# Optimization experiments

Hardware: AMD Instinct MI355X
Metric: run time of the kernel (lower is better)

Reference implementation:

```python
import jax, jax.numpy as jnp
import numpy as np

VOL = 128
FACTOR = 0.5 * VOL
N = 262144
LAT = 16
B = 8


def setup_inputs() -> dict:
    key = jax.random.key(0)
    ks = jax.random.split(key, 10)
    x = jax.random.normal(ks[0], (B, LAT), jnp.float32)
    inds = jax.random.randint(ks[1], (N, 3), 1, 126, dtype=jnp.int32)
    reference_values = jax.random.normal(ks[2], (N,), jnp.float32)
    # SIREN first layer: U(-1/in, 1/in)
    W0 = jax.random.uniform(ks[3], (LAT, 8), jnp.float32, -1.0 / LAT, 1.0 / LAT)
    b0 = jnp.zeros((8,), jnp.float32)
    # SIREN hidden layers (4 residual layers): U(-sqrt(6/in), sqrt(6/in))
    lim_h = float(np.sqrt(6.0 / 8.0))
    Wh = jax.random.uniform(ks[4], (4, 8, 8), jnp.float32, -lim_h, lim_h)
    bh = jnp.zeros((4, 8), jnp.float32)
    # final glorot-uniform layer: 8 -> 4N
    lim_f = float(np.sqrt(6.0 / (8.0 + 4.0 * N)))
    Wf = jax.random.uniform(ks[5], (8, 4 * N), jnp.float32, -lim_f, lim_f)
    bf = jnp.zeros((4 * N,), jnp.float32)
    return {"x": x, "W0": W0, "b0": b0, "Wh": Wh, "bh": bh, "Wf": Wf,
            "bf": bf, "reference_values": reference_values, "inds": inds}


def _siren_mlp(x, W0, b0, Wh, bh, Wf, bf):
    bf16 = jnp.bfloat16
    h = jnp.sin(30.0 * (x.astype(bf16) @ W0.astype(bf16) + b0.astype(bf16)))
    for i in range(Wh.shape[0]):  # 4 residual sine layers, 8-wide
        h = h + jnp.sin(h @ Wh[i].astype(bf16) + bh[i].astype(bf16))
    return h.astype(jnp.float32) @ Wf + bf  # [B, 4N], final layer in fp32


def reference(x, W0, b0, Wh, bh, Wf, bf, reference_values, inds):
    Bn = x.shape[0]
    out = _siren_mlp(x, W0, b0, Wh, bh, Wf, bf).reshape(Bn, N, 4)
    delta_coords, delta_values = out[..., :3], out[..., 3]
    # coords = stack(z,y,x reversed) normalized to [-1,1)
    coords_norm = (jnp.stack([inds[:, 2], inds[:, 1], inds[:, 0]], axis=1)
                   .astype(jnp.float32) - FACTOR) / FACTOR  # [N,3]
    values = reference_values + delta_values                 # [B,N]
    coords = FACTOR * (coords_norm[None] + delta_coords) + FACTOR  # [B,N,3]
    bposf = jnp.floor(coords)
    bposi = bposf.astype(jnp.int32)
    f = coords - bposf
    fx, fy, fz = f[..., 0], f[..., 1], f[..., 2]
    gx, gy, gz = 1.0 - fx, 1.0 - fy, 1.0 - fz
    # 8 trilinear weights, in the original concat order
    w = jnp.stack([gx * gy * gz, fx * gy * gz, gx * fy * gz, gx * gy * fz,
                   gx * fy * fz, fx * gy * fz, fx * fy * gz, fx * fy * fz],
                  axis=1)                                    # [B,8,N]
    bamp = (values[:, None, :] * w).reshape(Bn, 8 * N)
    offs = jnp.array([[0, 0, 0], [1, 0, 0], [0, 1, 0], [0, 0, 1],
                      [0, 1, 1], [1, 0, 1], [1, 1, 0], [1, 1, 1]], jnp.int32)
    bpos = (bposi[:, None, :, :] + offs[None, :, None, :]).reshape(Bn, 8 * N, 3)

    def scatter(pos, amp):
        return jnp.zeros((VOL, VOL, VOL), jnp.float32).at[
            pos[:, 2], pos[:, 1], pos[:, 0]].add(amp)

    grids = jax.vmap(scatter)(bpos, bamp)  # [B,128,128,128]
    return grids
```

## Files before the change

kernel.cpp:

```cpp
#include <hip/hip_runtime.h>
#include <math.h>

#define VOL   128
#define V2    (VOL*VOL)
#define V3    (VOL*VOL*VOL)
#define NPTS  262144
#define LATD  16
#define BATCH 8
#define FACTORF 64.0f
#define NBINS (VOL*VOL)
#define RZ 8
#define RY 4
#define REG_PER_B ((VOL/RZ)*(VOL/RY))
#define HALO_Z 13
#define HALO_Y 9
#define NRANGE (HALO_Z*HALO_Y)
#define FAR_CAP 8192

#define WS_HBUF    0u
#define WS_HIST    256u
#define WS_START   65792u
#define WS_RANK    131344u
#define WS_WGSUM   1179920u
#define WS_CTRL    1180432u
#define WS_FARLIST 1180464u
#define WS_COORDS  1737008u
#define WS_FULL    35291440u

__device__ __forceinline__ float bf16r(float x) {
    unsigned u = __float_as_uint(x);
    u = (u + 0x7fffu + ((u >> 16) & 1u)) & 0xffff0000u;
    return __uint_as_float(u);
}

__global__ void mlp_kernel(const float* __restrict__ x,
                           const float* __restrict__ W0,
                           const float* __restrict__ b0,
                           const float* __restrict__ Wh,
                           const float* __restrict__ bh,
                           float* __restrict__ hout) {
    int b = threadIdx.x;
    if (b >= BATCH) return;
    float xb[LATD];
    #pragma unroll
    for (int i = 0; i < LATD; ++i) xb[i] = bf16r(x[b*LATD + i]);
    float h[8];
    #pragma unroll
    for (int j = 0; j < 8; ++j) {
        float acc = 0.f;
        #pragma unroll
        for (int i = 0; i < LATD; ++i) acc += xb[i] * bf16r(W0[i*8 + j]);
        float t = bf16r(acc);
        t = bf16r(t + bf16r(b0[j]));
        t = bf16r(30.0f * t);
        h[j] = bf16r(sinf(t));
    }
    for (int l = 0; l < 4; ++l) {
        float nh[8];
        #pragma unroll
        for (int j = 0; j < 8; ++j) {
            float acc = 0.f;
            #pragma unroll
            for (int r = 0; r < 8; ++r) acc += h[r] * bf16r(Wh[(l*8 + r)*8 + j]);
            float t = bf16r(acc);
            t = bf16r(t + bf16r(bh[l*8 + j]));
            float s = bf16r(sinf(t));
            nh[j] = bf16r(h[j] + s);
        }
        #pragma unroll
        for (int j = 0; j < 8; ++j) h[j] = nh[j];
    }
    #pragma unroll
    for (int j = 0; j < 8; ++j) hout[b*8 + j] = h[j];
}

__global__ __launch_bounds__(256) void hist_rank_kernel(const int* __restrict__ inds,
                                                        unsigned* __restrict__ hist,
                                                        unsigned* __restrict__ rank) {
    int n = blockIdx.x * 256 + threadIdx.x;
    if (n >= NPTS) return;
    rank[n] = atomicAdd(&hist[inds[n*3]*VOL + inds[n*3+1]], 1u);
}

__global__ __launch_bounds__(256) void scanA_kernel(const unsigned* __restrict__ hist,
                                                    unsigned* __restrict__ wgsum) {
    __shared__ unsigned s[256];
    int t = threadIdx.x;
    s[t] = hist[blockIdx.x * 256 + t];
    __syncthreads();
    for (int off = 128; off > 0; off >>= 1) {
        if (t < off) s[t] += s[t + off];
        __syncthreads();
    }
    if (t == 0) wgsum[blockIdx.x] = s[0];
}
__global__ __launch_bounds__(64) void scanB_kernel(unsigned* __restrict__ wgsum,
                                                   unsigned* __restrict__ binstart,
                                                   unsigned* __restrict__ ctrl) {
    if (threadIdx.x == 0) {
        unsigned run = 0;
        for (int i = 0; i < 64; ++i) { unsigned v = wgsum[i]; wgsum[i] = run; run += v; }
        binstart[NBINS] = run;
        ctrl[0] = 0u; ctrl[1] = 0u;
    }
}
__global__ __launch_bounds__(256) void scanC_kernel(const unsigned* __restrict__ hist,
                                                    const unsigned* __restrict__ wgsum,
                                                    unsigned* __restrict__ binstart) {
    __shared__ unsigned s[256];
    int t = threadIdx.x;
    int idx = blockIdx.x * 256 + t;
    unsigned h = hist[idx];
    s[t] = h; __syncthreads();
    for (int off = 1; off < 256; off <<= 1) {
        unsigned v = (t >= off) ? s[t - off] : 0u;
        __syncthreads();
        s[t] += v;
        __syncthreads();
    }
    binstart[idx] = s[t] - h + wgsum[blockIdx.x];
}

__global__ __launch_bounds__(256) void coords_kernel(
    const float* __restrict__ Wf, const float* __restrict__ bfv_g,
    const float* __restrict__ rv, const int* __restrict__ inds,
    const float* __restrict__ hbuf, const unsigned* __restrict__ binstart,
    const unsigned* __restrict__ rank,
    unsigned* __restrict__ ctrl, unsigned* __restrict__ farlist,
    float4* __restrict__ coords_s)
{
    __shared__ float hs[64];
    if (threadIdx.x < 64) hs[threadIdx.x] = hbuf[threadIdx.x];
    __syncthreads();
    int n = blockIdx.x * 256 + threadIdx.x;
    if (n >= NPTS) return;
    int iz = inds[n*3], iy = inds[n*3+1], ix = inds[n*3+2];
    float cnx = ((float)ix - FACTORF) / FACTORF;
    float cny = ((float)iy - FACTORF) / FACTORF;
    float cnz = ((float)iz - FACTORF) / FACTORF;
    float val0 = rv[n];
    float4 bfv = ((const float4*)bfv_g)[n];
    float4 wf[8];
    #pragma unroll
    for (int r = 0; r < 8; ++r)
        wf[r] = ((const float4*)(Wf + (size_t)r * 4 * NPTS))[n];
    unsigned pos = binstart[iz*VOL + iy] + rank[n];
    #pragma unroll
    for (int b = 0; b < BATCH; ++b) {
        float o0 = bfv.x, o1 = bfv.y, o2 = bfv.z, o3 = bfv.w;
        #pragma unroll
        for (int r = 0; r < 8; ++r) {
            float hv = hs[b*8 + r];
            o0 = fmaf(hv, wf[r].x, o0);
            o1 = fmaf(hv, wf[r].y, o1);
            o2 = fmaf(hv, wf[r].z, o2);
            o3 = fmaf(hv, wf[r].w, o3);
        }
        float4 c;
        c.x = FACTORF * (cnx + o0) + FACTORF;
        c.y = FACTORF * (cny + o1) + FACTORF;
        c.z = FACTORF * (cnz + o2) + FACTORF;
        c.w = val0 + o3;
        coords_s[(size_t)b * NPTS + pos] = c;
        int bz = (int)floorf(c.z), by = (int)floorf(c.y);
        bool nearzy = ((unsigned)(bz - iz + 2) <= 4u) &&
                      ((unsigned)(by - iy + 2) <= 4u);
        if (!nearzy) {
            unsigned fp = atomicAdd(&ctrl[0], 1u);
            if (fp < FAR_CAP) farlist[fp] = (pos << 3) | (unsigned)b;
        }
    }
}

__global__ __launch_bounds__(256) void region_kernel(
    const float4* __restrict__ coords_s,
    const unsigned* __restrict__ binstart, float* __restrict__ out)
{
    __shared__ float tile[RZ*RY*VOL];
    __shared__ unsigned rstart[NRANGE];
    __shared__ unsigned rcum[NRANGE+1];
    __shared__ short rpz[NRANGE], rpy[NRANGE];
    int tid = threadIdx.x;
    int b   = blockIdx.x & 7;
    int rid = blockIdx.x >> 3;
    int z0 = (rid >> 5) * RZ, y0 = (rid & 31) * RY;

    for (int i = tid; i < RZ*RY*VOL; i += 256) tile[i] = 0.f;

    if (tid < NRANGE) {
        int zi = tid / HALO_Y, yi = tid - zi * HALO_Y;
        int zz = (z0 - 3 + zi) & (VOL-1);
        int yy = (y0 - 3 + yi) & (VOL-1);
        int base = zz * VOL + yy;
        unsigned s = binstart[base];
        rstart[tid] = s;
        rpz[tid] = (short)zz; rpy[tid] = (short)yy;
        rcum[tid+1] = binstart[base+1] - s;
    }
    if (tid == 0) rcum[0] = 0u;
    __syncthreads();
    for (int off = 1; off < NRANGE; off <<= 1) {
        unsigned v = 0u;
        if (tid < NRANGE && tid >= off) v = rcum[tid+1-off];
        __syncthreads();
        if (tid < NRANGE && tid >= off) rcum[tid+1] += v;
        __syncthreads();
    }
    unsigned total = rcum[NRANGE];

    const int ox[8] = {0,1,0,0,0,1,1,1};
    const int oy[8] = {0,0,1,0,1,0,1,1};
    const int oz[8] = {0,0,0,1,1,1,0,1};
    const float4* cb = coords_s + (size_t)b * NPTS;

    int r = 0;
    for (unsigned f = tid; f < total; f += 2048u) {
        float4 c[8]; int pz[8], py[8]; bool v[8];
        #pragma unroll
        for (int u = 0; u < 8; ++u) {
            unsigned fu = f + (unsigned)u * 256u;
            v[u] = fu < total;
            if (v[u]) {
                while (fu >= rcum[r+1]) ++r;
                unsigned j = rstart[r] + (fu - rcum[r]);
                c[u] = cb[j];
                pz[u] = rpz[r]; py[u] = rpy[r];
            }
        }
        #pragma unroll
        for (int u = 0; u < 8; ++u) {
            if (!v[u]) continue;
            float4 cc = c[u];
            float fxf = floorf(cc.x), fyf = floorf(cc.y), fzf = floorf(cc.z);
            int bx = (int)fxf, by = (int)fyf, bz = (int)fzf;
            bool nearzy = ((unsigned)(bz - pz[u] + 2) <= 4u) &&
                          ((unsigned)(by - py[u] + 2) <= 4u);
            if (!nearzy) continue;
            float fx = cc.x - fxf, fy = cc.y - fyf, fz = cc.z - fzf;
            float gx = 1.f - fx, gy = 1.f - fy, gz = 1.f - fz;
            float val = cc.w;
            float w[8] = {gx*gy*gz, fx*gy*gz, gx*fy*gz, gx*gy*fz,
                          gx*fy*fz, fx*gy*fz, fx*fy*gz, fx*fy*fz};
            #pragma unroll
            for (int o = 0; o < 8; ++o) {
                int Z = (bz + oz[o]) & 127, dz = Z - z0;
                if ((unsigned)dz >= RZ) continue;
                int Y = (by + oy[o]) & 127, dy = Y - y0;
                if ((unsigned)dy >= RY) continue;
                int X = (bx + ox[o]) & 127;
                atomicAdd(&tile[(dz << 9) + (dy << 7) + X], val * w[o]);
            }
        }
    }
    __syncthreads();
    size_t ob = (size_t)b * V3;
    for (int i = tid; i < RZ*RY*VOL; i += 256) {
        int lz = i >> 9, ly = (i >> 7) & (RY-1), lx = i & 127;
        out[ob + (size_t)(z0+lz)*V2 + (y0+ly)*VOL + lx] = tile[i];
    }
}

__global__ __launch_bounds__(256) void far_kernel(
    const float4* __restrict__ coords_s, const unsigned* __restrict__ ctrl,
    const unsigned* __restrict__ farlist, float* __restrict__ out)
{
    unsigned cnt = ctrl[0];
    if (cnt > FAR_CAP) cnt = FAR_CAP;
    const int ox[8] = {0,1,0,0,0,1,1,1};
    const int oy[8] = {0,0,1,0,1,0,1,1};
    const int oz[8] = {0,0,0,1,1,1,0,1};
    for (unsigned idx = blockIdx.x * 256 + threadIdx.x; idx < cnt;
         idx += gridDim.x * 256) {
        unsigned e = farlist[idx];
        unsigned pos = e >> 3;
        int b = (int)(e & 7u);
        float4 c = coords_s[(size_t)b * NPTS + pos];
        float fxf = floorf(c.x), fyf = floorf(c.y), fzf = floorf(c.z);
        int bx = (int)fxf, by = (int)fyf, bz = (int)fzf;
        float fx = c.x - fxf, fy = c.y - fyf, fz = c.z - fzf;
        float gx = 1.f - fx, gy = 1.f - fy, gz = 1.f - fz;
        float val = c.w;
        float w[8] = {gx*gy*gz, fx*gy*gz, gx*fy*gz, gx*gy*fz,
                      gx*fy*fz, fx*gy*fz, fx*fy*gz, fx*fy*fz};
        float* ob = out + (size_t)b * V3;
        #pragma unroll
        for (int o = 0; o < 8; ++o) {
            int Z = (bz + oz[o]) & (VOL-1);
            int Y = (by + oy[o]) & (VOL-1);
            int X = (bx + ox[o]) & (VOL-1);
            atomicAdd(ob + (size_t)Z*V2 + Y*VOL + X, val * w[o]);
        }
    }
}

__global__ __launch_bounds__(256) void scatter_fallback(
    const float* __restrict__ Wf, const float* __restrict__ bfv_g,
    const float* __restrict__ rv, const int* __restrict__ inds,
    const float* __restrict__ hbuf, float* __restrict__ out)
{
    __shared__ float hs[BATCH*8];
    if (threadIdx.x < BATCH*8) hs[threadIdx.x] = hbuf[threadIdx.x];
    __syncthreads();
    int n = blockIdx.x * blockDim.x + threadIdx.x;
    if (n >= NPTS) return;
    int iz = inds[n*3 + 0], iy = inds[n*3 + 1], ix = inds[n*3 + 2];
    float cnx = ((float)ix - FACTORF) / FACTORF;
    float cny = ((float)iy - FACTORF) / FACTORF;
    float cnz = ((float)iz - FACTORF) / FACTORF;
    float val0 = rv[n];
    float4 bfv = ((const float4*)bfv_g)[n];
    float4 wf[8];
    #pragma unroll
    for (int r = 0; r < 8; ++r)
        wf[r] = ((const float4*)(Wf + (size_t)r * 4 * NPTS))[n];
    static const int offs[8][3] = {{0,0,0},{1,0,0},{0,1,0},{0,0,1},
                                   {0,1,1},{1,0,1},{1,1,0},{1,1,1}};
    #pragma unroll
    for (int b = 0; b < BATCH; ++b) {
        float o0 = bfv.x, o1 = bfv.y, o2 = bfv.z, o3 = bfv.w;
        #pragma unroll
        for (int r = 0; r < 8; ++r) {
            float hv = hs[b*8 + r];
            o0 = fmaf(hv, wf[r].x, o0);
            o1 = fmaf(hv, wf[r].y, o1);
            o2 = fmaf(hv, wf[r].z, o2);
            o3 = fmaf(hv, wf[r].w, o3);
        }
        float cx = FACTORF * (cnx + o0) + FACTORF;
        float cy = FACTORF * (cny + o1) + FACTORF;
        float cz = FACTORF * (cnz + o2) + FACTORF;
        float val = val0 + o3;
        float fxf = floorf(cx), fyf = floorf(cy), fzf = floorf(cz);
        int bx = (int)fxf, by = (int)fyf, bz = (int)fzf;
        float fx = cx - fxf, fy = cy - fyf, fz = cz - fzf;
        float gx = 1.f - fx, gy = 1.f - fy, gz = 1.f - fz;
        float w[8] = {gx*gy*gz, fx*gy*gz, gx*fy*gz, gx*gy*fz,
                      gx*fy*fz, fx*gy*fz, fx*fy*gz, fx*fy*fz};
        float* ob = out + (size_t)b * V3;
        #pragma unroll
        for (int o = 0; o < 8; ++o) {
            int X = (bx + offs[o][0]) & (VOL-1);
            int Y = (by + offs[o][1]) & (VOL-1);
            int Z = (bz + offs[o][2]) & (VOL-1);
            atomicAdd(ob + (size_t)Z*V2 + Y*VOL + X, val * w[o]);
        }
    }
}

extern "C" void kernel_launch(void* const* d_in, const int* in_sizes, int n_in,
                              void* d_out, int out_size, void* d_ws, size_t ws_size,
                              hipStream_t stream) {
    const float* x    = (const float*)d_in[0];
    const float* W0   = (const float*)d_in[1];
    const float* b0   = (const float*)d_in[2];
    const float* Wh   = (const float*)d_in[3];
    const float* bh   = (const float*)d_in[4];
    const float* Wf   = (const float*)d_in[5];
    const float* bf   = (const float*)d_in[6];
    const float* rv   = (const float*)d_in[7];
    const int*   inds = (const int*)d_in[8];
    float* out = (float*)d_out;
    char*  ws  = (char*)d_ws;

    float*    hbuf     = (float*)(ws + WS_HBUF);
    unsigned* hist     = (unsigned*)(ws + WS_HIST);
    unsigned* binstart = (unsigned*)(ws + WS_START);
    unsigned* rank     = (unsigned*)(ws + WS_RANK);
    unsigned* wgsum    = (unsigned*)(ws + WS_WGSUM);
    unsigned* ctrl     = (unsigned*)(ws + WS_CTRL);
    unsigned* farlist  = (unsigned*)(ws + WS_FARLIST);
    float4*   coords_s = (float4*)(ws + WS_COORDS);

    mlp_kernel<<<1, 64, 0, stream>>>(x, W0, b0, Wh, bh, hbuf);

    if (ws_size >= (size_t)WS_FULL) {
        hipMemsetAsync(hist, 0, NBINS*4, stream);
        hist_rank_kernel<<<NPTS/256, 256, 0, stream>>>(inds, hist, rank);
        scanA_kernel<<<64, 256, 0, stream>>>(hist, wgsum);
        scanB_kernel<<<1, 64, 0, stream>>>(wgsum, binstart, ctrl);
        scanC_kernel<<<64, 256, 0, stream>>>(hist, wgsum, binstart);
        coords_kernel<<<NPTS/256, 256, 0, stream>>>(Wf, bf, rv, inds, hbuf,
                                                    binstart, rank,
                                                    ctrl, farlist, coords_s);
        region_kernel<<<REG_PER_B*BATCH, 256, 0, stream>>>(coords_s, binstart, out);
        far_kernel<<<8, 256, 0, stream>>>(coords_s, ctrl, farlist, out);
    } else {
        hipMemsetAsync(d_out, 0, (size_t)out_size * sizeof(float), stream);
        scatter_fallback<<<NPTS/256, 256, 0, stream>>>(Wf, bf, rv, inds, hbuf, out);
    }
}
```

Before: 188.3 us.

## Assign contiguous point ranges per thread and reorder region block mapping

Region blocks are now grouped by batch (batch = blockIdx>>9) instead of interleaving batches across adjacent blocks. Each thread processes a contiguous chunk of the flattened bin range, located with a binary search, rather than a strided interleave. This is meant to improve cache locality for the coordinate reads and reduce the per-element range-walk cost. The trade-off is that per-thread global loads are no longer coalesced across the wavefront, and adjacent threads hit the shared tile at more scattered addresses.

```diff
diff --git a/kernel.cpp b/kernel.cpp
--- a/kernel.cpp
+++ b/kernel.cpp
@@ -181,8 +181,8 @@
     __shared__ unsigned rcum[NRANGE+1];
     __shared__ short rpz[NRANGE], rpy[NRANGE];
     int tid = threadIdx.x;
-    int b   = blockIdx.x & 7;
-    int rid = blockIdx.x >> 3;
+    int b   = blockIdx.x >> 9;
+    int rid = blockIdx.x & 511;
     int z0 = (rid >> 5) * RZ, y0 = (rid & 31) * RY;
 
     for (int i = tid; i < RZ*RY*VOL; i += 256) tile[i] = 0.f;
@@ -213,14 +213,27 @@
     const int oz[8] = {0,0,0,1,1,1,0,1};
     const float4* cb = coords_s + (size_t)b * NPTS;
 
+    unsigned L  = (total + 255u) >> 8;
+    unsigned p0 = (unsigned)tid * L;
+    unsigned p1 = p0 + L < total ? p0 + L : total;
+
     int r = 0;
-    for (unsigned f = tid; f < total; f += 2048u) {
-        float4 c[8]; int pz[8], py[8]; bool v[8];
-        #pragma unroll
-        for (int u = 0; u < 8; ++u) {
-            unsigned fu = f + (unsigned)u * 256u;
-            v[u] = fu < total;
-            if (v[u]) {
+    if (p0 < total) {
+        int lo = 0, hi = NRANGE;
+        while (lo + 1 < hi) {
+            int mid = (lo + hi) >> 1;
+            if (rcum[mid] <= p0) lo = mid; else hi = mid;
+        }
+        r = lo;
+    }
+
+    for (unsigned base = p0; base < p1; base += 8u) {
+        unsigned cnt = (p1 - base < 8u) ? (p1 - base) : 8u;
+        float4 c[8]; int pz[8], py[8];
+        #pragma unroll
+        for (unsigned u = 0; u < 8; ++u) {
+            if (u < cnt) {
+                unsigned fu = base + u;
                 while (fu >= rcum[r+1]) ++r;
                 unsigned j = rstart[r] + (fu - rcum[r]);
                 c[u] = cb[j];
@@ -228,8 +241,8 @@
             }
         }
         #pragma unroll
-        for (int u = 0; u < 8; ++u) {
-            if (!v[u]) continue;
+        for (unsigned u = 0; u < 8; ++u) {
+            if (u >= cnt) continue;
             float4 cc = c[u];
             float fxf = floorf(cc.x), fyf = floorf(cc.y), fzf = floorf(cc.z);
             int bx = (int)fxf, by = (int)fyf, bz = (int)fzf;
```

Result: slower. 193.0 us (+2.5%).

## Process all batches per region block, reusing a precomputed shared point index list

Applied to the files above, without the earlier changes.

Each region block now loops over all 8 batch items instead of one block per (region, batch). It builds a flat shared-memory list of point indices with encoded halo offsets once, replacing the per-thread range search. It falls back to the old search when the list overflows. This amortizes the bin scan and lookup across batches, but cuts the grid eightfold, lowering occupancy and parallelism.

```diff
diff --git a/kernel.cpp b/kernel.cpp
--- a/kernel.cpp
+++ b/kernel.cpp
@@ -15,6 +15,7 @@
 #define HALO_Z 13
 #define HALO_Y 9
 #define NRANGE (HALO_Z*HALO_Y)
+#define JCAP 4096
 #define FAR_CAP 8192
 
 #define WS_HBUF    0u
@@ -172,20 +173,17 @@
     }
 }
 
-__global__ __launch_bounds__(256) void region_kernel(
+__global__ __launch_bounds__(256) void region8_kernel(
     const float4* __restrict__ coords_s,
     const unsigned* __restrict__ binstart, float* __restrict__ out)
 {
     __shared__ float tile[RZ*RY*VOL];
+    __shared__ unsigned jlist[JCAP];
     __shared__ unsigned rstart[NRANGE];
     __shared__ unsigned rcum[NRANGE+1];
-    __shared__ short rpz[NRANGE], rpy[NRANGE];
     int tid = threadIdx.x;
-    int b   = blockIdx.x & 7;
-    int rid = blockIdx.x >> 3;
+    int rid = blockIdx.x;
     int z0 = (rid >> 5) * RZ, y0 = (rid & 31) * RY;
-
-    for (int i = tid; i < RZ*RY*VOL; i += 256) tile[i] = 0.f;
 
     if (tid < NRANGE) {
         int zi = tid / HALO_Y, yi = tid - zi * HALO_Y;
@@ -194,7 +192,6 @@
         int base = zz * VOL + yy;
         unsigned s = binstart[base];
         rstart[tid] = s;
-        rpz[tid] = (short)zz; rpy[tid] = (short)yy;
         rcum[tid+1] = binstart[base+1] - s;
     }
     if (tid == 0) rcum[0] = 0u;
@@ -207,56 +204,102 @@
         __syncthreads();
     }
     unsigned total = rcum[NRANGE];
+    bool fits = total <= JCAP;
+
+    if (fits && tid < NRANGE) {
+        int zi = tid / HALO_Y, yi = tid - zi * HALO_Y;
+        unsigned meta = ((unsigned)zi << 22) | ((unsigned)yi << 26);
+        unsigned s = rstart[tid], o = rcum[tid], cnt = rcum[tid+1] - o;
+        for (unsigned k = 0; k < cnt; ++k)
+            jlist[o + k] = (s + k) | meta;
+    }
+    __syncthreads();
 
     const int ox[8] = {0,1,0,0,0,1,1,1};
     const int oy[8] = {0,0,1,0,1,0,1,1};
     const int oz[8] = {0,0,0,1,1,1,0,1};
-    const float4* cb = coords_s + (size_t)b * NPTS;
-
-    int r = 0;
-    for (unsigned f = tid; f < total; f += 2048u) {
-        float4 c[8]; int pz[8], py[8]; bool v[8];
-        #pragma unroll
-        for (int u = 0; u < 8; ++u) {
-            unsigned fu = f + (unsigned)u * 256u;
-            v[u] = fu < total;
-            if (v[u]) {
-                while (fu >= rcum[r+1]) ++r;
-                unsigned j = rstart[r] + (fu - rcum[r]);
-                c[u] = cb[j];
-                pz[u] = rpz[r]; py[u] = rpy[r];
+
+    for (int b = 0; b < BATCH; ++b) {
+        for (int i = tid; i < RZ*RY*VOL; i += 256) tile[i] = 0.f;
+        __syncthreads();
+        const float4* cb = coords_s + (size_t)b * NPTS;
+
+        if (fits) {
+            for (unsigned f = tid; f < total; f += 2048u) {
+                float4 c[8]; int pz[8], py[8]; bool v[8];
+                #pragma unroll
+                for (int u = 0; u < 8; ++u) {
+                    unsigned fu = f + (unsigned)u * 256u;
+                    v[u] = fu < total;
+                    if (v[u]) {
+                        unsigned e = jlist[fu];
+                        c[u] = cb[e & 0x3FFFFFu];
+                        pz[u] = (z0 - 3 + (int)((e >> 22) & 15u)) & (VOL-1);
+                        py[u] = (y0 - 3 + (int)((e >> 26) & 15u)) & (VOL-1);
+                    }
+                }
+                #pragma unroll
+                for (int u = 0; u < 8; ++u) {
+                    if (!v[u]) continue;
+                    float4 cc = c[u];
+                    float fxf = floorf(cc.x), fyf = floorf(cc.y), fzf = floorf(cc.z);
+                    int bx = (int)fxf, by = (int)fyf, bz = (int)fzf;
+                    bool nearzy = ((unsigned)(bz - pz[u] + 2) <= 4u) &&
+                                  ((unsigned)(by - py[u] + 2) <= 4u);
+                    if (!nearzy) continue;
+                    float fx = cc.x - fxf, fy = cc.y - fyf, fz = cc.z - fzf;
+                    float gx = 1.f - fx, gy = 1.f - fy, gz = 1.f - fz;
+                    float val = cc.w;
+                    float w[8] = {gx*gy*gz, fx*gy*gz, gx*fy*gz, gx*gy*fz,
+                                  gx*fy*fz, fx*gy*fz, fx*fy*gz, fx*fy*fz};
+                    #pragma unroll
+                    for (int o = 0; o < 8; ++o) {
+                        int Z = (bz + oz[o]) & 127, dz = Z - z0;
+                        if ((unsigned)dz >= RZ) continue;
+                        int Y = (by + oy[o]) & 127, dy = Y - y0;
+                        if ((unsigned)dy >= RY) continue;
+                        int X = (bx + ox[o]) & 127;
+                        atomicAdd(&tile[(dz << 9) + (dy << 7) + X], val * w[o]);
+                    }
+                }
             }
-        }
-        #pragma unroll
-        for (int u = 0; u < 8; ++u) {
-            if (!v[u]) continue;
-            float4 cc = c[u];
-            float fxf = floorf(cc.x), fyf = floorf(cc.y), fzf = floorf(cc.z);
-            int bx = (int)fxf, by = (int)fyf, bz = (int)fzf;
-            bool nearzy = ((unsigned)(bz - pz[u] + 2) <= 4u) &&
-                          ((unsigned)(by - py[u] + 2) <= 4u);
-            if (!nearzy) continue;
-            float fx = cc.x - fxf, fy = cc.y - fyf, fz = cc.z - fzf;
-            float gx = 1.f - fx, gy = 1.f - fy, gz = 1.f - fz;
-            float val = cc.w;
-            float w[8] = {gx*gy*gz, fx*gy*gz, gx*fy*gz, gx*gy*fz,
-                          gx*fy*fz, fx*gy*fz, fx*fy*gz, fx*fy*fz};
-            #pragma unroll
-            for (int o = 0; o < 8; ++o) {
-                int Z = (bz + oz[o]) & 127, dz = Z - z0;
-                if ((unsigned)dz >= RZ) continue;
-                int Y = (by + oy[o]) & 127, dy = Y - y0;
-                if ((unsigned)dy >= RY) continue;
-                int X = (bx + ox[o]) & 127;
-                atomicAdd(&tile[(dz << 9) + (dy << 7) + X], val * w[o]);
+        } else {
+            int r = 0;
+            for (unsigned f = tid; f < total; f += 256u) {
+                while (f >= rcum[r+1]) ++r;
+                unsigned j = rstart[r] + (f - rcum[r]);
+                int zi = r / HALO_Y, yi = r - zi * HALO_Y;
+                int pzv = (z0 - 3 + zi) & (VOL-1);
+                int pyv = (y0 - 3 + yi) & (VOL-1);
+                float4 cc = cb[j];
+                float fxf = floorf(cc.x), fyf = floorf(cc.y), fzf = floorf(cc.z);
+                int bx = (int)fxf, by = (int)fyf, bz = (int)fzf;
+                bool nearzy = ((unsigned)(bz - pzv + 2) <= 4u) &&
+                              ((unsigned)(by - pyv + 2) <= 4u);
+                if (!nearzy) continue;
+                float fx = cc.x - fxf, fy = cc.y - fyf, fz = cc.z - fzf;
+                float gx = 1.f - fx, gy = 1.f - fy, gz = 1.f - fz;
+                float val = cc.w;
+                float w[8] = {gx*gy*gz, fx*gy*gz, gx*fy*gz, gx*gy*fz,
+                              gx*fy*fz, fx*gy*fz, fx*fy*gz, fx*fy*fz};
+                #pragma unroll
+                for (int o = 0; o < 8; ++o) {
+                    int Z = (bz + oz[o]) & 127, dz = Z - z0;
+                    if ((unsigned)dz >= RZ) continue;
+                    int Y = (by + oy[o]) & 127, dy = Y - y0;
+                    if ((unsigned)dy >= RY) continue;
+                    int X = (bx + ox[o]) & 127;
+                    atomicAdd(&tile[(dz << 9) + (dy << 7) + X], val * w[o]);
+                }
             }
         }
-    }
-    __syncthreads();
-    size_t ob = (size_t)b * V3;
-    for (int i = tid; i < RZ*RY*VOL; i += 256) {
-        int lz = i >> 9, ly = (i >> 7) & (RY-1), lx = i & 127;
-        out[ob + (size_t)(z0+lz)*V2 + (y0+ly)*VOL + lx] = tile[i];
+        __syncthreads();
+        size_t ob = (size_t)b * V3;
+        for (int i = tid; i < RZ*RY*VOL; i += 256) {
+            int lz = i >> 9, ly = (i >> 7) & (RY-1), lx = i & 127;
+            out[ob + (size_t)(z0+lz)*V2 + (y0+ly)*VOL + lx] = tile[i];
+        }
+        __syncthreads();
     }
 }
 
@@ -382,7 +425,7 @@
         coords_kernel<<<NPTS/256, 256, 0, stream>>>(Wf, bf, rv, inds, hbuf,
                                                     binstart, rank,
                                                     ctrl, farlist, coords_s);
-        region_kernel<<<REG_PER_B*BATCH, 256, 0, stream>>>(coords_s, binstart, out);
+        region8_kernel<<<REG_PER_B, 256, 0, stream>>>(coords_s, binstart, out);
         far_kernel<<<8, 256, 0, stream>>>(coords_s, ctrl, farlist, out);
     } else {
         hipMemsetAsync(d_out, 0, (size_t)out_size * sizeof(float), stream);
```

Measured after the change: 191.4 us. Within noise of the previous version (+1.6%).

## Compress sorted coords to 16-bit fixed point and store far points directly

Applied to the files above, without the earlier changes.

Sorted per-batch coordinates are now packed as ushort4: x in 1/256 fixed point, y and z as 1/8192 offsets relative to the bin, and the value in fp16. This halves the intermediate buffer that the region kernel streams. The per-point rank array is replaced by an atomic cursor taken in the coords kernel, and far points are written as full float4 records so the far kernel no longer gathers from the coords buffer. The region kernel's block order now walks regions within one batch before moving on, which may change L2 locality. Quantizing coordinates and values adds rounding error compared with the fp32 reference.

```diff
diff --git a/kernel.cpp b/kernel.cpp
--- a/kernel.cpp
+++ b/kernel.cpp
@@ -1,5 +1,7 @@
 #include <hip/hip_runtime.h>
+#include <hip/hip_fp16.h>
 #include <math.h>
+#include <string.h>
 
 #define VOL   128
 #define V2    (VOL*VOL)
@@ -17,20 +19,29 @@
 #define NRANGE (HALO_Z*HALO_Y)
 #define FAR_CAP 8192
 
-#define WS_HBUF    0u
-#define WS_HIST    256u
-#define WS_START   65792u
-#define WS_RANK    131344u
-#define WS_WGSUM   1179920u
-#define WS_CTRL    1180432u
-#define WS_FARLIST 1180464u
-#define WS_COORDS  1737008u
-#define WS_FULL    35291440u
+#define WS_HBUF   0u
+#define WS_HIST   256u
+#define WS_START  65792u
+#define WS_CURSOR 131584u
+#define WS_WGSUM  197120u
+#define WS_CTRL   197376u
+#define WS_FARBUF 197408u
+#define WS_COORDC 328480u
+#define WS_FULL   17105696u
 
 __device__ __forceinline__ float bf16r(float x) {
     unsigned u = __float_as_uint(x);
     u = (u + 0x7fffu + ((u >> 16) & 1u)) & 0xffff0000u;
     return __uint_as_float(u);
+}
+__device__ __forceinline__ unsigned short f16bits(float v) {
+    __half h = __float2half_rn(v);
+    unsigned short us; memcpy(&us, &h, 2);
+    return us;
+}
+__device__ __forceinline__ float f16val(unsigned short us) {
+    __half h; memcpy(&h, &us, 2);
+    return __half2float(h);
 }
 
 __global__ void mlp_kernel(const float* __restrict__ x,
@@ -74,12 +85,11 @@
     for (int j = 0; j < 8; ++j) hout[b*8 + j] = h[j];
 }
 
-__global__ __launch_bounds__(256) void hist_rank_kernel(const int* __restrict__ inds,
-                                                        unsigned* __restrict__ hist,
-                                                        unsigned* __restrict__ rank) {
+__global__ __launch_bounds__(256) void hist_kernel(const int* __restrict__ inds,
+                                                   unsigned* __restrict__ hist) {
     int n = blockIdx.x * 256 + threadIdx.x;
     if (n >= NPTS) return;
-    rank[n] = atomicAdd(&hist[inds[n*3]*VOL + inds[n*3+1]], 1u);
+    atomicAdd(&hist[inds[n*3]*VOL + inds[n*3+1]], 1u);
 }
 
 __global__ __launch_bounds__(256) void scanA_kernel(const unsigned* __restrict__ hist,
@@ -106,7 +116,8 @@
 }
 __global__ __launch_bounds__(256) void scanC_kernel(const unsigned* __restrict__ hist,
                                                     const unsigned* __restrict__ wgsum,
-                                                    unsigned* __restrict__ binstart) {
+                                                    unsigned* __restrict__ binstart,
+                                                    unsigned* __restrict__ cursor) {
     __shared__ unsigned s[256];
     int t = threadIdx.x;
     int idx = blockIdx.x * 256 + t;
@@ -118,16 +129,17 @@
         s[t] += v;
         __syncthreads();
     }
-    binstart[idx] = s[t] - h + wgsum[blockIdx.x];
+    unsigned excl = s[t] - h + wgsum[blockIdx.x];
+    binstart[idx] = excl;
+    cursor[idx]   = excl;
 }
 
 __global__ __launch_bounds__(256) void coords_kernel(
     const float* __restrict__ Wf, const float* __restrict__ bfv_g,
     const float* __restrict__ rv, const int* __restrict__ inds,
-    const float* __restrict__ hbuf, const unsigned* __restrict__ binstart,
-    const unsigned* __restrict__ rank,
-    unsigned* __restrict__ ctrl, unsigned* __restrict__ farlist,
-    float4* __restrict__ coords_s)
+    const float* __restrict__ hbuf, unsigned* __restrict__ cursor,
+    unsigned* __restrict__ ctrl, float4* __restrict__ farbuf,
+    ushort4* __restrict__ coords_c)
 {
     __shared__ float hs[64];
     if (threadIdx.x < 64) hs[threadIdx.x] = hbuf[threadIdx.x];
@@ -144,7 +156,7 @@
     #pragma unroll
     for (int r = 0; r < 8; ++r)
         wf[r] = ((const float4*)(Wf + (size_t)r * 4 * NPTS))[n];
-    unsigned pos = binstart[iz*VOL + iy] + rank[n];
+    unsigned pos = atomicAdd(&cursor[iz*VOL + iy], 1u);
     #pragma unroll
     for (int b = 0; b < BATCH; ++b) {
         float o0 = bfv.x, o1 = bfv.y, o2 = bfv.z, o3 = bfv.w;
@@ -156,24 +168,31 @@
             o2 = fmaf(hv, wf[r].z, o2);
             o3 = fmaf(hv, wf[r].w, o3);
         }
-        float4 c;
-        c.x = FACTORF * (cnx + o0) + FACTORF;
-        c.y = FACTORF * (cny + o1) + FACTORF;
-        c.z = FACTORF * (cnz + o2) + FACTORF;
-        c.w = val0 + o3;
-        coords_s[(size_t)b * NPTS + pos] = c;
-        int bz = (int)floorf(c.z), by = (int)floorf(c.y);
+        float cx = FACTORF * (cnx + o0) + FACTORF;
+        float cy = FACTORF * (cny + o1) + FACTORF;
+        float cz = FACTORF * (cnz + o2) + FACTORF;
+        float val = val0 + o3;
+        int bz = (int)floorf(cz), by = (int)floorf(cy);
         bool nearzy = ((unsigned)(bz - iz + 2) <= 4u) &&
                       ((unsigned)(by - iy + 2) <= 4u);
-        if (!nearzy) {
+        ushort4 e;
+        if (nearzy) {
+            e.x = (unsigned short)fminf(fmaxf(fmaf(cx + 8.f, 256.f, 0.5f), 0.f), 65535.f);
+            e.y = (unsigned short)fminf(fmaf(cy - (float)iy + 2.f, 8192.f, 0.5f), 40959.f);
+            e.z = (unsigned short)fminf(fmaf(cz - (float)iz + 2.f, 8192.f, 0.5f), 40959.f);
+            e.w = f16bits(val);
+        } else {
+            e.x = 0; e.y = 0xFFFFu; e.z = 0; e.w = 0;
             unsigned fp = atomicAdd(&ctrl[0], 1u);
-            if (fp < FAR_CAP) farlist[fp] = (pos << 3) | (unsigned)b;
-        }
+            if (fp < FAR_CAP)
+                farbuf[fp] = make_float4(cx, cy, cz + 256.0f * (float)b, val);
+        }
+        coords_c[(size_t)b * NPTS + pos] = e;
     }
 }
 
 __global__ __launch_bounds__(256) void region_kernel(
-    const float4* __restrict__ coords_s,
+    const ushort4* __restrict__ coords_c,
     const unsigned* __restrict__ binstart, float* __restrict__ out)
 {
     __shared__ float tile[RZ*RY*VOL];
@@ -181,8 +200,8 @@
     __shared__ unsigned rcum[NRANGE+1];
     __shared__ short rpz[NRANGE], rpy[NRANGE];
     int tid = threadIdx.x;
-    int b   = blockIdx.x & 7;
-    int rid = blockIdx.x >> 3;
+    int b   = blockIdx.x >> 9;
+    int rid = blockIdx.x & 511;
     int z0 = (rid >> 5) * RZ, y0 = (rid & 31) * RY;
 
     for (int i = tid; i < RZ*RY*VOL; i += 256) tile[i] = 0.f;
@@ -211,11 +230,11 @@
     const int ox[8] = {0,1,0,0,0,1,1,1};
     const int oy[8] = {0,0,1,0,1,0,1,1};
     const int oz[8] = {0,0,0,1,1,1,0,1};
-    const float4* cb = coords_s + (size_t)b * NPTS;
+    const ushort4* cb = coords_c + (size_t)b * NPTS;
 
     int r = 0;
     for (unsigned f = tid; f < total; f += 2048u) {
-        float4 c[8]; int pz[8], py[8]; bool v[8];
+        ushort4 e[8]; int pz[8], py[8]; bool v[8];
         #pragma unroll
         for (int u = 0; u < 8; ++u) {
             unsigned fu = f + (unsigned)u * 256u;
@@ -223,22 +242,22 @@
             if (v[u]) {
                 while (fu >= rcum[r+1]) ++r;
                 unsigned j = rstart[r] + (fu - rcum[r]);
-                c[u] = cb[j];
+                e[u] = cb[j];
                 pz[u] = rpz[r]; py[u] = rpy[r];
             }
         }
         #pragma unroll
         for (int u = 0; u < 8; ++u) {
-            if (!v[u]) continue;
-            float4 cc = c[u];
-            float fxf = floorf(cc.x), fyf = floorf(cc.y), fzf = floorf(cc.z);
+            if (!v[u] || e[u].y == 0xFFFFu) continue;
+            int piz = pz[u], piy = py[u];
+            float cx = (float)e[u].x * (1.f/256.f) - 8.f;
+            float cy = (float)piy + (float)e[u].y * (1.f/8192.f) - 2.f;
+            float cz = (float)piz + (float)e[u].z * (1.f/8192.f) - 2.f;
+            float val = f16val(e[u].w);
+            float fxf = floorf(cx), fyf = floorf(cy), fzf = floorf(cz);
             int bx = (int)fxf, by = (int)fyf, bz = (int)fzf;
-            bool nearzy = ((unsigned)(bz - pz[u] + 2) <= 4u) &&
-                          ((unsigned)(by - py[u] + 2) <= 4u);
-            if (!nearzy) continue;
-            float fx = cc.x - fxf, fy = cc.y - fyf, fz = cc.z - fzf;
+            float fx = cx - fxf, fy = cy - fyf, fz = cz - fzf;
             float gx = 1.f - fx, gy = 1.f - fy, gz = 1.f - fz;
-            float val = cc.w;
             float w[8] = {gx*gy*gz, fx*gy*gz, gx*fy*gz, gx*gy*fz,
                           gx*fy*fz, fx*gy*fz, fx*fy*gz, fx*fy*fz};
             #pragma unroll
@@ -261,8 +280,8 @@
 }
 
 __global__ __launch_bounds__(256) void far_kernel(
-    const float4* __restrict__ coords_s, const unsigned* __restrict__ ctrl,
-    const unsigned* __restrict__ farlist, float* __restrict__ out)
+    const unsigned* __restrict__ ctrl, const float4* __restrict__ farbuf,
+    float* __restrict__ out)
 {
     unsigned cnt = ctrl[0];
     if (cnt > FAR_CAP) cnt = FAR_CAP;
@@ -271,13 +290,12 @@
     const int oz[8] = {0,0,0,1,1,1,0,1};
     for (unsigned idx = blockIdx.x * 256 + threadIdx.x; idx < cnt;
          idx += gridDim.x * 256) {
-        unsigned e = farlist[idx];
-        unsigned pos = e >> 3;
-        int b = (int)(e & 7u);
-        float4 c = coords_s[(size_t)b * NPTS + pos];
-        float fxf = floorf(c.x), fyf = floorf(c.y), fzf = floorf(c.z);
+        float4 c = farbuf[idx];
+        int b = (int)floorf((c.z + 8.0f) * (1.0f/256.0f));
+        float cz = c.z - 256.0f * (float)b;
+        float fxf = floorf(c.x), fyf = floorf(c.y), fzf = floorf(cz);
         int bx = (int)fxf, by = (int)fyf, bz = (int)fzf;
-        float fx = c.x - fxf, fy = c.y - fyf, fz = c.z - fzf;
+        float fx = c.x - fxf, fy = c.y - fyf, fz = cz - fzf;
         float gx = 1.f - fx, gy = 1.f - fy, gz = 1.f - fz;
         float val = c.w;
         float w[8] = {gx*gy*gz, fx*gy*gz, gx*fy*gz, gx*gy*fz,
@@ -365,25 +383,24 @@
     float*    hbuf     = (float*)(ws + WS_HBUF);
     unsigned* hist     = (unsigned*)(ws + WS_HIST);
     unsigned* binstart = (unsigned*)(ws + WS_START);
-    unsigned* rank     = (unsigned*)(ws + WS_RANK);
+    unsigned* cursor   = (unsigned*)(ws + WS_CURSOR);
     unsigned* wgsum    = (unsigned*)(ws + WS_WGSUM);
     unsigned* ctrl     = (unsigned*)(ws + WS_CTRL);
-    unsigned* farlist  = (unsigned*)(ws + WS_FARLIST);
-    float4*   coords_s = (float4*)(ws + WS_COORDS);
+    float4*   farbuf   = (float4*)(ws + WS_FARBUF);
+    ushort4*  coords_c = (ushort4*)(ws + WS_COORDC);
 
     mlp_kernel<<<1, 64, 0, stream>>>(x, W0, b0, Wh, bh, hbuf);
 
     if (ws_size >= (size_t)WS_FULL) {
         hipMemsetAsync(hist, 0, NBINS*4, stream);
-        hist_rank_kernel<<<NPTS/256, 256, 0, stream>>>(inds, hist, rank);
+        hist_kernel<<<NPTS/256, 256, 0, stream>>>(inds, hist);
         scanA_kernel<<<64, 256, 0, stream>>>(hist, wgsum);
         scanB_kernel<<<1, 64, 0, stream>>>(wgsum, binstart, ctrl);
-        scanC_kernel<<<64, 256, 0, stream>>>(hist, wgsum, binstart);
+        scanC_kernel<<<64, 256, 0, stream>>>(hist, wgsum, binstart, cursor);
         coords_kernel<<<NPTS/256, 256, 0, stream>>>(Wf, bf, rv, inds, hbuf,
-                                                    binstart, rank,
-                                                    ctrl, farlist, coords_s);
-        region_kernel<<<REG_PER_B*BATCH, 256, 0, stream>>>(coords_s, binstart, out);
-        far_kernel<<<8, 256, 0, stream>>>(coords_s, ctrl, farlist, out);
+                                                    cursor, ctrl, farbuf, coords_c);
+        region_kernel<<<REG_PER_B*BATCH, 256, 0, stream>>>(coords_c, binstart, out);
+        far_kernel<<<8, 256, 0, stream>>>(ctrl, farbuf, out);
     } else {
         hipMemsetAsync(d_out, 0, (size_t)out_size * sizeof(float), stream);
         scatter_fallback<<<NPTS/256, 256, 0, stream>>>(Wf, bf, rv, inds, hbuf, out);
```

Result: slower. 198.4 us (+5.4%).
